# Kernel optimization log

Hardware: AMD Instinct MI355X
Metric: run time of the kernel (lower is better)

The kernel has to match this reference:

```python
import jax, jax.numpy as jnp
import numpy as np

B = 512     # graphs
NPG = 128   # nodes per graph
EPG = 2048  # edges per graph (avg degree 16)
IN = 128
HID = 128
K = 64      # ceil(0.5 * 128), SAGPooling ratio=0.5


def setup_inputs() -> dict:
    key = jax.random.key(0)
    ks = jax.random.split(key, 8)
    n_total = B * NPG
    x = jax.random.normal(ks[0], (n_total, IN), dtype=jnp.float32)
    # intra-graph random edges (PyG batching: edges never cross graphs)
    g = jnp.repeat(jnp.arange(B, dtype=jnp.int32), EPG)
    src = g * NPG + jax.random.randint(ks[1], (B * EPG,), 0, NPG, dtype=jnp.int32)
    dst = g * NPG + jax.random.randint(ks[2], (B * EPG,), 0, NPG, dtype=jnp.int32)
    edge_index = jnp.stack([src, dst], axis=0)
    batch = jnp.repeat(jnp.arange(B, dtype=jnp.int32), NPG)
    # params (glorot-ish scaling)
    W1 = jax.random.normal(ks[3], (IN, HID), dtype=jnp.float32) / np.sqrt(IN)
    b1 = jnp.zeros((HID,), dtype=jnp.float32)
    Ws = jax.random.normal(ks[4], (HID, 1), dtype=jnp.float32) / np.sqrt(HID)
    bs = jnp.zeros((1,), dtype=jnp.float32)
    Wlin = jax.random.normal(ks[5], (HID, HID), dtype=jnp.float32) / np.sqrt(HID)
    blin = jnp.zeros((HID,), dtype=jnp.float32)
    return {"x": x, "edge_index": edge_index, "batch": batch,
            "W1": W1, "b1": b1, "Ws": Ws, "bs": bs, "Wlin": Wlin, "blin": blin}


def _gcn_conv(x, src, dst, W, b, n):
    # PyG GCNConv: add self loops, symmetric deg^-1/2 norm, aggregate src->dst
    h = x @ W  # [n, out]
    loop = jnp.arange(n, dtype=src.dtype)
    s = jnp.concatenate([src, loop])
    d = jnp.concatenate([dst, loop])
    deg = jax.ops.segment_sum(jnp.ones(d.shape[0], dtype=x.dtype), d, num_segments=n)
    norm = jax.lax.rsqrt(deg)[s] * jax.lax.rsqrt(deg)[d]  # deg >= 1 via self loops
    msg = h[s] * norm[:, None]
    return jax.ops.segment_sum(msg, d, num_segments=n) + b


def reference(x, edge_index, batch, W1, b1, Ws, bs, Wlin, blin):
    n = x.shape[0]
    src, dst = edge_index[0], edge_index[1]
    # conv1 + relu
    h = jax.nn.relu(_gcn_conv(x, src, dst, W1, b1, n))  # [n, HID]
    # SAGPooling: score via GCNConv(HID -> 1)
    score = _gcn_conv(h, src, dst, Ws, bs, n)[:, 0]  # [n]
    # per-graph top-k on raw score (graphs are uniform NPG nodes -> dense top_k)
    score2 = score.reshape(B, NPG)
    top_v, top_i = jax.lax.top_k(score2, K)  # [B, K]
    h3 = h.reshape(B, NPG, HID)
    h_kept = jnp.take_along_axis(h3, top_i[:, :, None], axis=1)  # [B, K, HID]
    h_kept = h_kept * jnp.tanh(top_v)[:, :, None]  # x[perm] * tanh(score[perm])
    # global_mean_pool over kept nodes of each graph
    pooled = h_kept.mean(axis=1)  # [B, HID]
    return pooled @ Wlin + blin
```

## Files before the change

kernel.cpp:

```cpp
#include <hip/hip_runtime.h>
#include <math.h>

#define NPG  128
#define HID  128
#define KSEL 64
#define NT   256
#define CSRCAP 2432

typedef __attribute__((ext_vector_type(8))) __bf16 bfrag;
typedef __attribute__((ext_vector_type(4))) float f4;

__global__ __launch_bounds__(64) void wsplit_kernel(const float* __restrict__ W1,
                                                    bfrag* __restrict__ whi,
                                                    bfrag* __restrict__ wlo)
{
    const int b = blockIdx.x;
    const int ks = b >> 3, ct = b & 7;
    const int lane = threadIdx.x;
    const int n = lane & 15, quad = lane >> 4;
    bfrag h, l;
#pragma unroll
    for (int j = 0; j < 8; ++j) {
        const int k = ks * 32 + quad * 8 + j;
        float w = W1[k * HID + ct * 16 + n];
        __bf16 hh = (__bf16)w;
        h[j] = hh;
        l[j] = (__bf16)(w - (float)hh);
    }
    whi[b * 64 + lane] = h;
    wlo[b * 64 + lane] = l;
}

__global__ __launch_bounds__(NT, 2) void sagpool_fused(
    const float* __restrict__ x,
    const int*   __restrict__ esrc,
    const int*   __restrict__ edst,
    const bfrag* __restrict__ whi,
    const bfrag* __restrict__ wlo,
    const float* __restrict__ b1,
    const float* __restrict__ Ws,
    const float* __restrict__ bsp,
    const float* __restrict__ Wlin,
    const float* __restrict__ blin,
    float* __restrict__ out,
    int epg)
{
    __shared__ float Hs[NPG + 1][HID];
    __shared__ unsigned char srcs[CSRCAP];
    __shared__ int   degl[NPG];
    __shared__ int   off[NPG + 1];
    __shared__ int   cur[NPG];
    __shared__ float rsl[NPG];
    __shared__ float spl[NPG + 1];
    __shared__ float scl[NPG];
    __shared__ float wgt[NPG];
    __shared__ float pooled[HID];
    __shared__ float pp[2 * HID];
    __shared__ int   wsum[2];

    const int g = blockIdx.x, t = threadIdx.x;
    const int node0 = g * NPG;
    const long e0 = (long)g * epg;
    const int lane = t & 63, wv = t >> 6;

    int es[8], ed[8];
#pragma unroll
    for (int i = 0; i < 8; ++i) {
        int e = i * NT + t;
        es[i] = esrc[e0 + e] - node0;
        ed[i] = edst[e0 + e] - node0;
    }
    if (t < NPG) degl[t] = 0;
    if (t < HID) Hs[NPG][t] = 0.f;
    for (int i = t; i < CSRCAP / 4; i += NT)
        reinterpret_cast<int*>(srcs)[i] = (int)0x80808080;
    __syncthreads();

#pragma unroll
    for (int i = 0; i < 8; ++i) atomicAdd(&degl[ed[i]], 1);
    __syncthreads();

    int pc = 0;
    if (t < NPG) {
        int dg = degl[t];
        rsl[t] = rsqrtf((float)(dg + 1));
        pc = (dg + 3) & ~3;
    }
    int vscan = pc;
#pragma unroll
    for (int d = 1; d < 64; d <<= 1) {
        int u = __shfl_up(vscan, (unsigned)d, 64);
        if (lane >= d) vscan += u;
    }
    if (t < NPG && lane == 63) wsum[wv] = vscan;
    __syncthreads();
    if (t < NPG) {
        int inc = vscan + ((wv == 1) ? wsum[0] : 0);
        int ex = inc - pc;
        off[t] = ex; cur[t] = ex;
        if (t == NPG - 1) off[NPG] = inc;
    }
    __syncthreads();

#pragma unroll
    for (int i = 0; i < 8; ++i) {
        int slot = atomicAdd(&cur[ed[i]], 1);
        srcs[slot] = (unsigned char)es[i];
    }

    {
        const int mrow = lane & 15, quad = lane >> 4;
        f4 acc[2][8];
#pragma unroll
        for (int rt = 0; rt < 2; ++rt)
#pragma unroll
            for (int ct = 0; ct < 8; ++ct) {
                acc[rt][ct].x = 0.f; acc[rt][ct].y = 0.f;
                acc[rt][ct].z = 0.f; acc[rt][ct].w = 0.f;
            }

        const float* xw = x + (long)(node0 + wv * 32) * HID;
#pragma unroll
        for (int ks = 0; ks < 4; ++ks) {
            bfrag ah[2], al[2];
#pragma unroll
            for (int rt = 0; rt < 2; ++rt) {
                const float* xr = xw + (rt * 16 + mrow) * HID + ks * 32 + quad * 8;
                float4 v0 = *reinterpret_cast<const float4*>(xr);
                float4 v1 = *reinterpret_cast<const float4*>(xr + 4);
                float xv[8] = {v0.x, v0.y, v0.z, v0.w, v1.x, v1.y, v1.z, v1.w};
#pragma unroll
                for (int j = 0; j < 8; ++j) {
                    __bf16 hh = (__bf16)xv[j];
                    ah[rt][j] = hh;
                    al[rt][j] = (__bf16)(xv[j] - (float)hh);
                }
            }
#pragma unroll
            for (int ct = 0; ct < 8; ++ct) {
                bfrag bh = whi[(ks * 8 + ct) * 64 + lane];
                bfrag bl = wlo[(ks * 8 + ct) * 64 + lane];
#pragma unroll
                for (int rt = 0; rt < 2; ++rt) {
                    acc[rt][ct] = __builtin_amdgcn_mfma_f32_16x16x32_bf16(ah[rt], bh, acc[rt][ct], 0, 0, 0);
                    acc[rt][ct] = __builtin_amdgcn_mfma_f32_16x16x32_bf16(al[rt], bh, acc[rt][ct], 0, 0, 0);
                    acc[rt][ct] = __builtin_amdgcn_mfma_f32_16x16x32_bf16(ah[rt], bl, acc[rt][ct], 0, 0, 0);
                    acc[rt][ct] = __builtin_amdgcn_mfma_f32_16x16x32_bf16(al[rt], bl, acc[rt][ct], 0, 0, 0);
                }
            }
        }
#pragma unroll
        for (int rt = 0; rt < 2; ++rt)
#pragma unroll
            for (int reg = 0; reg < 4; ++reg) {
                const int m = wv * 32 + rt * 16 + quad * 4 + reg;
                const float rs = rsl[m];
#pragma unroll
                for (int ct = 0; ct < 8; ++ct)
                    Hs[m][ct * 16 + mrow] = acc[rt][ct][reg] * rs;
            }
    }
    __syncthreads();

    {
        const int hh = lane >> 5, c4 = lane & 31;
        float4 ga[16];
#pragma unroll
        for (int p = 0; p < 16; ++p) {
            int n = wv * 32 + 2 * p + hh;
            int ob = off[n], pcnt = off[n + 1] - ob;
            float4 a = *reinterpret_cast<const float4*>(&Hs[n][c4 * 4]);
            for (int jc = 0; jc < pcnt; jc += 4) {
                unsigned idx4 = *reinterpret_cast<const unsigned*>(&srcs[ob + jc]);
                int s0 = idx4 & 255, s1 = (idx4 >> 8) & 255,
                    s2 = (idx4 >> 16) & 255, s3 = (idx4 >> 24);
                float4 v0 = *reinterpret_cast<const float4*>(&Hs[s0][c4 * 4]);
                float4 v1 = *reinterpret_cast<const float4*>(&Hs[s1][c4 * 4]);
                float4 v2 = *reinterpret_cast<const float4*>(&Hs[s2][c4 * 4]);
                float4 v3 = *reinterpret_cast<const float4*>(&Hs[s3][c4 * 4]);
                a.x += v0.x + v1.x + v2.x + v3.x;
                a.y += v0.y + v1.y + v2.y + v3.y;
                a.z += v0.z + v1.z + v2.z + v3.z;
                a.w += v0.w + v1.w + v2.w + v3.w;
            }
            ga[p] = a;
        }
        __syncthreads();
        float4 b1v = *reinterpret_cast<const float4*>(&b1[c4 * 4]);
#pragma unroll
        for (int p = 0; p < 16; ++p) {
            int n = wv * 32 + 2 * p + hh;
            float r = rsl[n];
            float4 hv;
            hv.x = fmaxf(ga[p].x * r + b1v.x, 0.f);
            hv.y = fmaxf(ga[p].y * r + b1v.y, 0.f);
            hv.z = fmaxf(ga[p].z * r + b1v.z, 0.f);
            hv.w = fmaxf(ga[p].w * r + b1v.w, 0.f);
            *reinterpret_cast<float4*>(&Hs[n][c4 * 4]) = hv;
        }
    }
    __syncthreads();

    if (t < NPG) {
        float s = 0.f;
        for (int kk = 0; kk < 32; ++kk) {
            int k = (kk + t) & 31;
            float4 hv = *reinterpret_cast<const float4*>(&Hs[t][k * 4]);
            float4 wsv = *reinterpret_cast<const float4*>(&Ws[k * 4]);
            s += hv.x * wsv.x + hv.y * wsv.y + hv.z * wsv.z + hv.w * wsv.w;
        }
        spl[t] = rsl[t] * s;
        if (t == 0) spl[NPG] = 0.f;
    }
    __syncthreads();

    if (t < NPG) {
        int ob = off[t], pcnt = off[t + 1] - ob;
        float sc = spl[t];
        for (int jc = 0; jc < pcnt; jc += 4) {
            unsigned idx4 = *reinterpret_cast<const unsigned*>(&srcs[ob + jc]);
            sc += spl[idx4 & 255] + spl[(idx4 >> 8) & 255]
                + spl[(idx4 >> 16) & 255] + spl[idx4 >> 24];
        }
        scl[t] = rsl[t] * sc + bsp[0];
    }
    __syncthreads();

    if (t < NPG) {
        float v = scl[t];
        int rank = 0;
        for (int j = 0; j < NPG; ++j) {
            float u = scl[j];
            rank += (u > v || (u == v && j < t)) ? 1 : 0;
        }
        wgt[t] = (rank < KSEL) ? tanhf(v) * (1.0f / KSEL) : 0.f;
    }
    __syncthreads();

    {
        int c = t & 127, hf = t >> 7;
        float s = 0.f;
        for (int r = hf * 64; r < hf * 64 + 64; ++r)
            s += wgt[r] * Hs[r][c];
        pp[t] = s;
    }
    __syncthreads();
    if (t < HID) pooled[t] = pp[t] + pp[t + 128];
    __syncthreads();

    {
        int c = t & 127, hf = t >> 7;
        float s = 0.f;
        for (int k = hf * 64; k < hf * 64 + 64; ++k)
            s += pooled[k] * Wlin[k * HID + c];
        pp[t] = s;
    }
    __syncthreads();
    if (t < HID)
        out[(long)g * HID + t] = pp[t] + pp[t + 128] + blin[t];
}

extern "C" void kernel_launch(void* const* d_in, const int* in_sizes, int n_in,
                              void* d_out, int out_size, void* d_ws, size_t ws_size,
                              hipStream_t stream) {
    const float* x    = (const float*)d_in[0];
    const int*   ei   = (const int*)  d_in[1];
    const float* W1   = (const float*)d_in[3];
    const float* b1   = (const float*)d_in[4];
    const float* Ws   = (const float*)d_in[5];
    const float* bs   = (const float*)d_in[6];
    const float* Wlin = (const float*)d_in[7];
    const float* blin = (const float*)d_in[8];
    float* out = (float*)d_out;

    const int E = in_sizes[1] / 2;
    const int nnodes = in_sizes[0] / HID;
    const int B = nnodes / NPG;
    const int epg = E / B;

    bfrag* whi = reinterpret_cast<bfrag*>(d_ws);
    bfrag* wlo = whi + 32 * 64;

    wsplit_kernel<<<32, 64, 0, stream>>>(W1, whi, wlo);
    sagpool_fused<<<B, NT, 0, stream>>>(x, ei, ei + E, whi, wlo, b1, Ws, bs,
                                        Wlin, blin, out, epg);
}
```

Before: 121.4 us.

## Replace CSR gather aggregation with dense adjacency MFMA and register-resident epilogue

Replaces the CSR build and the per-node shared-memory gather with a packed 4-bit dense adjacency-count matrix. The neighbour aggregation becomes a bf16 MFMA matmul (A·H, with H split into hi/lo bf16 parts). Degrees, score projection, score aggregation and the pooled weighted sum now use the MFMA accumulator registers directly, with shuffle reductions instead of shared-memory passes, and the x loads are hoisted before the graph build. This removes scattered LDS gathers, the prefix scan and several barriers, but adds dense matmul work and relies on 4-bit edge counts (at most 15 duplicate edges per node pair) and split-bf16 accuracy.

```diff
diff --git a/kernel.cpp b/kernel.cpp
--- a/kernel.cpp
+++ b/kernel.cpp
@@ -5,10 +5,18 @@
 #define HID  128
 #define KSEL 64
 #define NT   256
-#define CSRCAP 2432
+#define HS   132
+#define AS   17
 
 typedef __attribute__((ext_vector_type(8))) __bf16 bfrag;
 typedef __attribute__((ext_vector_type(4))) float f4;
+
+static __device__ __forceinline__ __bf16 us2bf(unsigned short u) {
+    union { unsigned short s; __bf16 b; } x; x.s = u; return x.b;
+}
+static __device__ __forceinline__ unsigned short bf2us(__bf16 b) {
+    union { unsigned short s; __bf16 b; } x; x.b = b; return x.s;
+}
 
 __global__ __launch_bounds__(64) void wsplit_kernel(const float* __restrict__ W1,
                                                     bfrag* __restrict__ whi,
@@ -45,23 +53,19 @@
     float* __restrict__ out,
     int epg)
 {
-    __shared__ float Hs[NPG + 1][HID];
-    __shared__ unsigned char srcs[CSRCAP];
-    __shared__ int   degl[NPG];
-    __shared__ int   off[NPG + 1];
-    __shared__ int   cur[NPG];
-    __shared__ float rsl[NPG];
-    __shared__ float spl[NPG + 1];
-    __shared__ float scl[NPG];
-    __shared__ float wgt[NPG];
-    __shared__ float pooled[HID];
-    __shared__ float pp[2 * HID];
-    __shared__ int   wsum[2];
+    __shared__ __align__(16) unsigned HpT[HID * HS];
+    __shared__ __align__(16) unsigned AdjN[NPG * AS];
+    __shared__ __align__(16) float rsl[NPG];
+    __shared__ __align__(16) float spl[NPG];
+    __shared__ __align__(16) float scl[NPG];
+    __shared__ __align__(16) float wgt[NPG];
+    __shared__ __align__(16) float pp[4 * HID];
 
     const int g = blockIdx.x, t = threadIdx.x;
     const int node0 = g * NPG;
     const long e0 = (long)g * epg;
     const int lane = t & 63, wv = t >> 6;
+    const int n16 = lane & 15, quad = lane >> 4;
 
     int es[8], ed[8];
 #pragma unroll
@@ -70,159 +74,197 @@
         es[i] = esrc[e0 + e] - node0;
         ed[i] = edst[e0 + e] - node0;
     }
-    if (t < NPG) degl[t] = 0;
-    if (t < HID) Hs[NPG][t] = 0.f;
-    for (int i = t; i < CSRCAP / 4; i += NT)
-        reinterpret_cast<int*>(srcs)[i] = (int)0x80808080;
-    __syncthreads();
-
-#pragma unroll
-    for (int i = 0; i < 8; ++i) atomicAdd(&degl[ed[i]], 1);
-    __syncthreads();
-
-    int pc = 0;
+    float4 xv[16];
+    {
+        const float* xw = x + (long)(node0 + wv * 32) * HID;
+#pragma unroll
+        for (int rt = 0; rt < 2; ++rt)
+#pragma unroll
+            for (int ks = 0; ks < 4; ++ks) {
+                const float* xr = xw + (rt * 16 + n16) * HID + ks * 32 + quad * 8;
+                xv[(rt * 4 + ks) * 2]     = *reinterpret_cast<const float4*>(xr);
+                xv[(rt * 4 + ks) * 2 + 1] = *reinterpret_cast<const float4*>(xr + 4);
+            }
+    }
+    float b1v[8], wsv[8];
+#pragma unroll
+    for (int ct = 0; ct < 8; ++ct) {
+        b1v[ct] = b1[ct * 16 + n16];
+        wsv[ct] = Ws[ct * 16 + n16];
+    }
+    const float bsv = bsp[0];
+
+    for (int i = t; i < NPG * AS; i += NT) AdjN[i] = 0u;
+    __syncthreads();
+#pragma unroll
+    for (int i = 0; i < 8; ++i)
+        atomicAdd(&AdjN[ed[i] * AS + (es[i] >> 3)], 1u << ((es[i] & 7) * 4));
+    __syncthreads();
+
     if (t < NPG) {
-        int dg = degl[t];
-        rsl[t] = rsqrtf((float)(dg + 1));
-        pc = (dg + 3) & ~3;
-    }
-    int vscan = pc;
-#pragma unroll
-    for (int d = 1; d < 64; d <<= 1) {
-        int u = __shfl_up(vscan, (unsigned)d, 64);
-        if (lane >= d) vscan += u;
-    }
-    if (t < NPG && lane == 63) wsum[wv] = vscan;
-    __syncthreads();
+        unsigned* row = &AdjN[t * AS];
+        row[t >> 3] += 1u << ((t & 7) * 4);
+        unsigned sum = 0;
+#pragma unroll
+        for (int w = 0; w < 16; ++w) {
+            unsigned u = row[w];
+            unsigned b = (u & 0x0F0F0F0Fu) + ((u >> 4) & 0x0F0F0F0Fu);
+            sum += (b * 0x01010101u) >> 24;
+        }
+        rsl[t] = rsqrtf((float)sum);
+    }
+    __syncthreads();
+
+    bfrag ah[8], al[8];
+#pragma unroll
+    for (int r = 0; r < 8; ++r) {
+        float4 a = xv[2 * r], b = xv[2 * r + 1];
+        float vv[8] = {a.x, a.y, a.z, a.w, b.x, b.y, b.z, b.w};
+#pragma unroll
+        for (int j = 0; j < 8; ++j) {
+            __bf16 hb = (__bf16)vv[j];
+            ah[r][j] = hb;
+            al[r][j] = (__bf16)(vv[j] - (float)hb);
+        }
+    }
+    f4 acc[2][8];
+#pragma unroll
+    for (int rt = 0; rt < 2; ++rt)
+#pragma unroll
+        for (int ct = 0; ct < 8; ++ct) {
+            acc[rt][ct].x = 0.f; acc[rt][ct].y = 0.f;
+            acc[rt][ct].z = 0.f; acc[rt][ct].w = 0.f;
+        }
+#pragma unroll
+    for (int ks = 0; ks < 4; ++ks)
+#pragma unroll
+        for (int ct = 0; ct < 8; ++ct) {
+            bfrag bh = whi[(ks * 8 + ct) * 64 + lane];
+            bfrag bl = wlo[(ks * 8 + ct) * 64 + lane];
+#pragma unroll
+            for (int rt = 0; rt < 2; ++rt) {
+                const int r = rt * 4 + ks;
+                acc[rt][ct] = __builtin_amdgcn_mfma_f32_16x16x32_bf16(ah[r], bh, acc[rt][ct], 0, 0, 0);
+                acc[rt][ct] = __builtin_amdgcn_mfma_f32_16x16x32_bf16(al[r], bh, acc[rt][ct], 0, 0, 0);
+                acc[rt][ct] = __builtin_amdgcn_mfma_f32_16x16x32_bf16(ah[r], bl, acc[rt][ct], 0, 0, 0);
+                acc[rt][ct] = __builtin_amdgcn_mfma_f32_16x16x32_bf16(al[r], bl, acc[rt][ct], 0, 0, 0);
+            }
+        }
+
+#pragma unroll
+    for (int rt = 0; rt < 2; ++rt) {
+        const int mb = wv * 32 + rt * 16 + quad * 4;
+        f4 rs4 = *reinterpret_cast<const f4*>(&rsl[mb]);
+#pragma unroll
+        for (int ct = 0; ct < 8; ++ct) {
+            uint4 st;
+            unsigned pw[4];
+#pragma unroll
+            for (int reg = 0; reg < 4; ++reg) {
+                float v = acc[rt][ct][reg] * rs4[reg];
+                __bf16 hb = (__bf16)v;
+                __bf16 lb = (__bf16)(v - (float)hb);
+                pw[reg] = ((unsigned)bf2us(hb) << 16) | (unsigned)bf2us(lb);
+            }
+            st.x = pw[0]; st.y = pw[1]; st.z = pw[2]; st.w = pw[3];
+            *reinterpret_cast<uint4*>(&HpT[(ct * 16 + n16) * HS + mb]) = st;
+        }
+    }
+    __syncthreads();
+
+    f4 hacc[2][8];
+#pragma unroll
+    for (int mt = 0; mt < 2; ++mt)
+#pragma unroll
+        for (int ct = 0; ct < 8; ++ct) {
+            hacc[mt][ct].x = 0.f; hacc[mt][ct].y = 0.f;
+            hacc[mt][ct].z = 0.f; hacc[mt][ct].w = 0.f;
+        }
+#pragma unroll
+    for (int ks = 0; ks < 4; ++ks) {
+        bfrag af[2];
+#pragma unroll
+        for (int mt = 0; mt < 2; ++mt) {
+            unsigned w = AdjN[(wv * 32 + mt * 16 + n16) * AS + ks * 4 + quad];
+#pragma unroll
+            for (int j = 0; j < 8; ++j)
+                af[mt][j] = (__bf16)(float)((w >> (4 * j)) & 15u);
+        }
+#pragma unroll
+        for (int ct = 0; ct < 8; ++ct) {
+            const unsigned* bp = &HpT[(ct * 16 + n16) * HS + ks * 32 + quad * 8];
+            uint4 w0 = *reinterpret_cast<const uint4*>(bp);
+            uint4 w1 = *reinterpret_cast<const uint4*>(bp + 4);
+            unsigned ww[8] = {w0.x, w0.y, w0.z, w0.w, w1.x, w1.y, w1.z, w1.w};
+            bfrag bh, bl;
+#pragma unroll
+            for (int j = 0; j < 8; ++j) {
+                bh[j] = us2bf((unsigned short)(ww[j] >> 16));
+                bl[j] = us2bf((unsigned short)(ww[j] & 0xFFFFu));
+            }
+#pragma unroll
+            for (int mt = 0; mt < 2; ++mt) {
+                hacc[mt][ct] = __builtin_amdgcn_mfma_f32_16x16x32_bf16(af[mt], bh, hacc[mt][ct], 0, 0, 0);
+                hacc[mt][ct] = __builtin_amdgcn_mfma_f32_16x16x32_bf16(af[mt], bl, hacc[mt][ct], 0, 0, 0);
+            }
+        }
+    }
+
+    f4 rsm[2];
+#pragma unroll
+    for (int mt = 0; mt < 2; ++mt)
+        rsm[mt] = *reinterpret_cast<const f4*>(&rsl[wv * 32 + mt * 16 + quad * 4]);
+#pragma unroll
+    for (int mt = 0; mt < 2; ++mt)
+#pragma unroll
+        for (int ct = 0; ct < 8; ++ct)
+#pragma unroll
+            for (int reg = 0; reg < 4; ++reg)
+                hacc[mt][ct][reg] = fmaxf(hacc[mt][ct][reg] * rsm[mt][reg] + b1v[ct], 0.f);
+
+    {
+        float dot[2][4];
+#pragma unroll
+        for (int mt = 0; mt < 2; ++mt)
+#pragma unroll
+            for (int reg = 0; reg < 4; ++reg) dot[mt][reg] = 0.f;
+#pragma unroll
+        for (int ct = 0; ct < 8; ++ct)
+#pragma unroll
+            for (int mt = 0; mt < 2; ++mt)
+#pragma unroll
+                for (int reg = 0; reg < 4; ++reg)
+                    dot[mt][reg] += hacc[mt][ct][reg] * wsv[ct];
+#pragma unroll
+        for (int d = 1; d < 16; d <<= 1)
+#pragma unroll
+            for (int mt = 0; mt < 2; ++mt)
+#pragma unroll
+                for (int reg = 0; reg < 4; ++reg)
+                    dot[mt][reg] += __shfl_xor(dot[mt][reg], d, 64);
+        if (n16 == 0) {
+#pragma unroll
+            for (int mt = 0; mt < 2; ++mt)
+#pragma unroll
+                for (int reg = 0; reg < 4; ++reg)
+                    spl[wv * 32 + mt * 16 + quad * 4 + reg] = rsm[mt][reg] * dot[mt][reg];
+        }
+    }
+    __syncthreads();
+
     if (t < NPG) {
-        int inc = vscan + ((wv == 1) ? wsum[0] : 0);
-        int ex = inc - pc;
-        off[t] = ex; cur[t] = ex;
-        if (t == NPG - 1) off[NPG] = inc;
-    }
-    __syncthreads();
-
-#pragma unroll
-    for (int i = 0; i < 8; ++i) {
-        int slot = atomicAdd(&cur[ed[i]], 1);
-        srcs[slot] = (unsigned char)es[i];
-    }
-
-    {
-        const int mrow = lane & 15, quad = lane >> 4;
-        f4 acc[2][8];
-#pragma unroll
-        for (int rt = 0; rt < 2; ++rt)
-#pragma unroll
-            for (int ct = 0; ct < 8; ++ct) {
-                acc[rt][ct].x = 0.f; acc[rt][ct].y = 0.f;
-                acc[rt][ct].z = 0.f; acc[rt][ct].w = 0.f;
-            }
-
-        const float* xw = x + (long)(node0 + wv * 32) * HID;
-#pragma unroll
-        for (int ks = 0; ks < 4; ++ks) {
-            bfrag ah[2], al[2];
-#pragma unroll
-            for (int rt = 0; rt < 2; ++rt) {
-                const float* xr = xw + (rt * 16 + mrow) * HID + ks * 32 + quad * 8;
-                float4 v0 = *reinterpret_cast<const float4*>(xr);
-                float4 v1 = *reinterpret_cast<const float4*>(xr + 4);
-                float xv[8] = {v0.x, v0.y, v0.z, v0.w, v1.x, v1.y, v1.z, v1.w};
-#pragma unroll
-                for (int j = 0; j < 8; ++j) {
-                    __bf16 hh = (__bf16)xv[j];
-                    ah[rt][j] = hh;
-                    al[rt][j] = (__bf16)(xv[j] - (float)hh);
-                }
-            }
-#pragma unroll
-            for (int ct = 0; ct < 8; ++ct) {
-                bfrag bh = whi[(ks * 8 + ct) * 64 + lane];
-                bfrag bl = wlo[(ks * 8 + ct) * 64 + lane];
-#pragma unroll
-                for (int rt = 0; rt < 2; ++rt) {
-                    acc[rt][ct] = __builtin_amdgcn_mfma_f32_16x16x32_bf16(ah[rt], bh, acc[rt][ct], 0, 0, 0);
-                    acc[rt][ct] = __builtin_amdgcn_mfma_f32_16x16x32_bf16(al[rt], bh, acc[rt][ct], 0, 0, 0);
-                    acc[rt][ct] = __builtin_amdgcn_mfma_f32_16x16x32_bf16(ah[rt], bl, acc[rt][ct], 0, 0, 0);
-                    acc[rt][ct] = __builtin_amdgcn_mfma_f32_16x16x32_bf16(al[rt], bl, acc[rt][ct], 0, 0, 0);
-                }
-            }
-        }
-#pragma unroll
-        for (int rt = 0; rt < 2; ++rt)
-#pragma unroll
-            for (int reg = 0; reg < 4; ++reg) {
-                const int m = wv * 32 + rt * 16 + quad * 4 + reg;
-                const float rs = rsl[m];
-#pragma unroll
-                for (int ct = 0; ct < 8; ++ct)
-                    Hs[m][ct * 16 + mrow] = acc[rt][ct][reg] * rs;
-            }
-    }
-    __syncthreads();
-
-    {
-        const int hh = lane >> 5, c4 = lane & 31;
-        float4 ga[16];
-#pragma unroll
-        for (int p = 0; p < 16; ++p) {
-            int n = wv * 32 + 2 * p + hh;
-            int ob = off[n], pcnt = off[n + 1] - ob;
-            float4 a = *reinterpret_cast<const float4*>(&Hs[n][c4 * 4]);
-            for (int jc = 0; jc < pcnt; jc += 4) {
-                unsigned idx4 = *reinterpret_cast<const unsigned*>(&srcs[ob + jc]);
-                int s0 = idx4 & 255, s1 = (idx4 >> 8) & 255,
-                    s2 = (idx4 >> 16) & 255, s3 = (idx4 >> 24);
-                float4 v0 = *reinterpret_cast<const float4*>(&Hs[s0][c4 * 4]);
-                float4 v1 = *reinterpret_cast<const float4*>(&Hs[s1][c4 * 4]);
-                float4 v2 = *reinterpret_cast<const float4*>(&Hs[s2][c4 * 4]);
-                float4 v3 = *reinterpret_cast<const float4*>(&Hs[s3][c4 * 4]);
-                a.x += v0.x + v1.x + v2.x + v3.x;
-                a.y += v0.y + v1.y + v2.y + v3.y;
-                a.z += v0.z + v1.z + v2.z + v3.z;
-                a.w += v0.w + v1.w + v2.w + v3.w;
-            }
-            ga[p] = a;
-        }
-        __syncthreads();
-        float4 b1v = *reinterpret_cast<const float4*>(&b1[c4 * 4]);
-#pragma unroll
-        for (int p = 0; p < 16; ++p) {
-            int n = wv * 32 + 2 * p + hh;
-            float r = rsl[n];
-            float4 hv;
-            hv.x = fmaxf(ga[p].x * r + b1v.x, 0.f);
-            hv.y = fmaxf(ga[p].y * r + b1v.y, 0.f);
-            hv.z = fmaxf(ga[p].z * r + b1v.z, 0.f);
-            hv.w = fmaxf(ga[p].w * r + b1v.w, 0.f);
-            *reinterpret_cast<float4*>(&Hs[n][c4 * 4]) = hv;
-        }
-    }
-    __syncthreads();
-
-    if (t < NPG) {
-        float s = 0.f;
-        for (int kk = 0; kk < 32; ++kk) {
-            int k = (kk + t) & 31;
-            float4 hv = *reinterpret_cast<const float4*>(&Hs[t][k * 4]);
-            float4 wsv = *reinterpret_cast<const float4*>(&Ws[k * 4]);
-            s += hv.x * wsv.x + hv.y * wsv.y + hv.z * wsv.z + hv.w * wsv.w;
-        }
-        spl[t] = rsl[t] * s;
-        if (t == 0) spl[NPG] = 0.f;
-    }
-    __syncthreads();
-
-    if (t < NPG) {
-        int ob = off[t], pcnt = off[t + 1] - ob;
-        float sc = spl[t];
-        for (int jc = 0; jc < pcnt; jc += 4) {
-            unsigned idx4 = *reinterpret_cast<const unsigned*>(&srcs[ob + jc]);
-            sc += spl[idx4 & 255] + spl[(idx4 >> 8) & 255]
-                + spl[(idx4 >> 16) & 255] + spl[idx4 >> 24];
-        }
-        scl[t] = rsl[t] * sc + bsp[0];
+        const unsigned* row = &AdjN[t * AS];
+        float sc = 0.f;
+#pragma unroll
+        for (int w = 0; w < 16; ++w) {
+            unsigned u = row[w];
+            const float* sp = &spl[w * 8];
+            sc += (float)(u & 15u)         * sp[0] + (float)((u >> 4)  & 15u) * sp[1]
+                + (float)((u >> 8)  & 15u) * sp[2] + (float)((u >> 12) & 15u) * sp[3]
+                + (float)((u >> 16) & 15u) * sp[4] + (float)((u >> 20) & 15u) * sp[5]
+                + (float)((u >> 24) & 15u) * sp[6] + (float)(u >> 28)         * sp[7];
+        }
+        scl[t] = rsl[t] * sc + bsv;
     }
     __syncthreads();
 
@@ -238,25 +280,46 @@
     __syncthreads();
 
     {
-        int c = t & 127, hf = t >> 7;
-        float s = 0.f;
-        for (int r = hf * 64; r < hf * 64 + 64; ++r)
-            s += wgt[r] * Hs[r][c];
-        pp[t] = s;
-    }
-    __syncthreads();
-    if (t < HID) pooled[t] = pp[t] + pp[t + 128];
+        float p[8];
+        f4 wm[2];
+#pragma unroll
+        for (int mt = 0; mt < 2; ++mt)
+            wm[mt] = *reinterpret_cast<const f4*>(&wgt[wv * 32 + mt * 16 + quad * 4]);
+#pragma unroll
+        for (int ct = 0; ct < 8; ++ct) {
+            float s = 0.f;
+#pragma unroll
+            for (int mt = 0; mt < 2; ++mt)
+#pragma unroll
+                for (int reg = 0; reg < 4; ++reg)
+                    s += wm[mt][reg] * hacc[mt][ct][reg];
+            p[ct] = s;
+        }
+#pragma unroll
+        for (int d = 16; d < 64; d <<= 1)
+#pragma unroll
+            for (int ct = 0; ct < 8; ++ct)
+                p[ct] += __shfl_xor(p[ct], d, 64);
+        if (quad == 0) {
+#pragma unroll
+            for (int ct = 0; ct < 8; ++ct)
+                pp[wv * HID + ct * 16 + n16] = p[ct];
+        }
+    }
+    __syncthreads();
+    if (t < NPG)
+        scl[t] = pp[t] + pp[HID + t] + pp[2 * HID + t] + pp[3 * HID + t];
     __syncthreads();
 
     {
-        int c = t & 127, hf = t >> 7;
+        const int c = t & 127, hf = t >> 7;
         float s = 0.f;
         for (int k = hf * 64; k < hf * 64 + 64; ++k)
-            s += pooled[k] * Wlin[k * HID + c];
+            s += scl[k] * Wlin[k * HID + c];
         pp[t] = s;
     }
     __syncthreads();
-    if (t < HID)
+    if (t < NPG)
         out[(long)g * HID + t] = pp[t] + pp[t + 128] + blin[t];
 }
 
```

After: 111.8 us. -7.9%, faster.
